# Optimization experiments

Hardware: AMD Instinct MI355X
Metric: run time of the kernel (lower is better)

The kernel has to match this reference:

```python
import jax, jax.numpy as jnp
import numpy as np

NUM_INPUTS = 256
NUM_OUTPUTS = 256
BATCH = 1024


def build_lhs(ni: int, no: int) -> jnp.ndarray:
    """Constraint matrix of the bipartite flow graph.

    Edge ordering follows the torch code: for output o, for input j -> column o*ni + j.
    Rows 0..ni-1: flow conservation at each input node (sum of outgoing flows = x_i).
    Rows ni..ni+no-1: equality constraints flow(e1) - flow(e2) = 0 for the
    per-output equal_edges pair chosen by in_idx = round(o*ni/no).
    """
    E = ni * no
    lhs = np.zeros((ni + no, E), dtype=np.float32)
    for i in range(ni):
        lhs[i, np.arange(no) * ni + i] = 1.0
    for o in range(no):
        in_idx = round(o * ni / no)
        a = in_idx % ni
        b = (in_idx + 1) % ni
        lhs[ni + o, o * ni + a] += 1.0
        lhs[ni + o, o * ni + b] -= 1.0
    return jnp.asarray(lhs)


def setup_inputs() -> dict:
    key = jax.random.key(0)
    k1, k2 = jax.random.split(key)
    xs = jax.random.normal(k1, (BATCH, NUM_INPUTS), dtype=jnp.float32)
    param = jax.random.normal(k2, (NUM_INPUTS * NUM_OUTPUTS,), dtype=jnp.float32)
    lhs = build_lhs(NUM_INPUTS, NUM_OUTPUTS)
    return {"xs": xs, "param": param, "lhs": lhs}


def reference(xs, param, lhs):
    """Batched constrained flow solve.

    Per sample: f* = argmin ||f - c||^2 s.t. lhs @ f = rhs, with
    c = softplus(param) (edge capacities) and rhs = [x; 0].
    Closed form via KKT: f* = c + lhs^T (lhs lhs^T)^{-1} (rhs - lhs c).
    Outputs are the total inflow at each output node. The torch module solves
    this per sample in a Python loop; here it is vectorized over the batch.
    """
    B = xs.shape[0]
    ni = NUM_INPUTS
    no = NUM_OUTPUTS
    c = jax.nn.softplus(param)                                      # [E]
    rhs = jnp.concatenate([xs, jnp.zeros((B, no), xs.dtype)], 1)    # [B, C]
    M = lhs @ lhs.T                                                 # [C, C] small gram
    d = rhs - (lhs @ c)[None, :]                                    # [B, C]
    lam = jnp.linalg.solve(M, d.T).T                                # [B, C] multipliers
    flow = c[None, :] + lam @ lhs                                   # [B, E]
    # edges grouped by output: column o*ni + j -> output o gets sum over j
    return flow.reshape(B, no, ni).sum(-1)                          # [B, no]
```

## Files before the change

### kernel.cpp

```cpp
#include <hip/hip_runtime.h>
#include <math.h>

#define NI 256
#define NO 256
#define BATCH 1024


__device__ __forceinline__ float softplus_f(float x) {
    return fmaxf(x, 0.0f) + log1pf(expf(-fabsf(x)));
}

__device__ __forceinline__ float block_reduce_256(float v, float* lds) {
    #pragma unroll
    for (int off = 32; off > 0; off >>= 1)
        v += __shfl_down(v, off, 64);
    const int lane = threadIdx.x & 63;
    const int wave = threadIdx.x >> 6;
    if (lane == 0) lds[wave] = v;
    __syncthreads();
    float t = 0.0f;
    if (threadIdx.x < 4) t = lds[threadIdx.x];
    t += __shfl_down(t, 2, 64);
    t += __shfl_down(t, 1, 64);
    if (threadIdx.x == 0) lds[0] = t;
    __syncthreads();
    return lds[0];
}

__global__ __launch_bounds__(256) void reduce_kernel(const float* __restrict__ xs,
                                                     const float* __restrict__ param,
                                                     float* __restrict__ ws) {
    __shared__ float lds[4];
    const int bid = blockIdx.x;
    const int tid = threadIdx.x;
    float v;
    if (bid < NO) {
        v = softplus_f(param[bid * NI + tid]);
    } else {
        v = xs[(bid - NO) * NI + tid];
    }
    const float s = block_reduce_256(v, lds);
    if (tid == 0) ws[bid] = s;
}

__global__ __launch_bounds__(256) void out_kernel(const float* __restrict__ ws,
                                                  float* __restrict__ out) {
    __shared__ float lds[4];
    const int b = blockIdx.x;
    const int o = threadIdx.x;
    const float Co = ws[o];
    const float total = block_reduce_256(Co, lds);
    const float Sx = ws[NO + b];
    out[b * NO + o] = Co + (Sx - total) * (1.0f / (float)NO);
}

extern "C" void kernel_launch(void* const* d_in, const int* in_sizes, int n_in,
                              void* d_out, int out_size, void* d_ws, size_t ws_size,
                              hipStream_t stream) {
    const float* xs    = (const float*)d_in[0];
    const float* param = (const float*)d_in[1];
    float* out = (float*)d_out;
    float* ws  = (float*)d_ws;

    reduce_kernel<<<NO + BATCH, 256, 0, stream>>>(xs, param, ws);
    out_kernel<<<BATCH, 256, 0, stream>>>(ws, out);
}
```

Before: 164.8 us.

## Fuse reduce and output kernels into one cooperative launch with grid sync

Merges the two kernels into a single cooperative kernel: each block reduces its xs row (and the first 256 blocks also reduce softplus(param) rows), then a grid-wide barrier precedes the output computation. This removes one kernel launch and the inter-kernel gap. The cost is a grid sync across 1024 blocks, which requires all of them to be co-resident, and the cooperative launch path's own overhead. Each block still re-reduces the 256 column sums after the barrier.

After: 230.6 us. 39.9% more time.

```diff
diff --git a/kernel.cpp b/kernel.cpp
--- a/kernel.cpp
+++ b/kernel.cpp
@@ -1,9 +1,12 @@
 #include <hip/hip_runtime.h>
+#include <hip/hip_cooperative_groups.h>
 #include <math.h>
 
 #define NI 256
 #define NO 256
 #define BATCH 1024
+
+namespace cg = cooperative_groups;
 
 
 __device__ __forceinline__ float softplus_f(float x) {
@@ -27,31 +30,32 @@
     return lds[0];
 }
 
-__global__ __launch_bounds__(256) void reduce_kernel(const float* __restrict__ xs,
-                                                     const float* __restrict__ param,
-                                                     float* __restrict__ ws) {
-    __shared__ float lds[4];
-    const int bid = blockIdx.x;
-    const int tid = threadIdx.x;
-    float v;
-    if (bid < NO) {
-        v = softplus_f(param[bid * NI + tid]);
-    } else {
-        v = xs[(bid - NO) * NI + tid];
-    }
-    const float s = block_reduce_256(v, lds);
-    if (tid == 0) ws[bid] = s;
-}
-
-__global__ __launch_bounds__(256) void out_kernel(const float* __restrict__ ws,
-                                                  float* __restrict__ out) {
+__global__ __launch_bounds__(256, 4) void fused_kernel(const float* __restrict__ xs,
+                                                       const float* __restrict__ param,
+                                                       float* __restrict__ out,
+                                                       float* __restrict__ ws) {
     __shared__ float lds[4];
     const int b = blockIdx.x;
-    const int o = threadIdx.x;
-    const float Co = ws[o];
+    const int tid = threadIdx.x;
+
+    if (b < NO) {
+        const float c = softplus_f(param[b * NI + tid]);
+        const float s = block_reduce_256(c, lds);
+        if (tid == 0) ws[b] = s;
+        __syncthreads();
+    }
+    {
+        const float x = xs[b * NI + tid];
+        const float s = block_reduce_256(x, lds);
+        if (tid == 0) ws[NO + b] = s;
+    }
+
+    cg::this_grid().sync();
+
+    const float Co = ws[tid];
     const float total = block_reduce_256(Co, lds);
     const float Sx = ws[NO + b];
-    out[b * NO + o] = Co + (Sx - total) * (1.0f / (float)NO);
+    out[b * NO + tid] = Co + (Sx - total) * (1.0f / (float)NO);
 }
 
 extern "C" void kernel_launch(void* const* d_in, const int* in_sizes, int n_in,
@@ -62,6 +66,7 @@
     float* out = (float*)d_out;
     float* ws  = (float*)d_ws;
 
-    reduce_kernel<<<NO + BATCH, 256, 0, stream>>>(xs, param, ws);
-    out_kernel<<<BATCH, 256, 0, stream>>>(ws, out);
+    void* args[] = { (void*)&xs, (void*)&param, (void*)&out, (void*)&ws };
+    hipLaunchCooperativeKernel((void*)fused_kernel, dim3(BATCH), dim3(256),
+                               args, 0, stream);
 }
```
